# Kernel optimization log

Measured on AMD Instinct MI355X. Metric: run time of the kernel, lower is better.

Reference implementation:

```python
import jax, jax.numpy as jnp
import numpy as np

FLOW_NUM = 2048
H = 64  # lstm_output_dim
NOISE_DIM = 3


def _w(key, shape, s=0.08):
    return (jax.random.normal(key, shape, dtype=jnp.float32) * s)


def setup_inputs() -> dict:
    key = jax.random.key(0)
    ks = jax.random.split(key, 20)
    d = {
        "noise": jax.random.normal(ks[0], (FLOW_NUM, NOISE_DIM), dtype=jnp.float32),
        "w_ih0": _w(ks[1], (4 * H, NOISE_DIM)),
        "w_hh0": _w(ks[2], (4 * H, H)),
        "b_ih0": _w(ks[3], (4 * H,)),
        "b_hh0": _w(ks[4], (4 * H,)),
        "w_ih1": _w(ks[5], (4 * H, H)),
        "w_hh1": _w(ks[6], (4 * H, H)),
        "b_ih1": _w(ks[7], (4 * H,)),
        "b_hh1": _w(ks[8], (4 * H,)),
        "w_ih2": _w(ks[9], (4 * H, H)),
        "w_hh2": _w(ks[10], (4 * H, H)),
        "b_ih2": _w(ks[11], (4 * H,)),
        "b_hh2": _w(ks[12], (4 * H,)),
        "fc1_w": _w(ks[13], (32, H)),
        "fc1_b": _w(ks[14], (32,)),
        "fc2_w": _w(ks[15], (16, 32)),
        "fc2_b": _w(ks[16], (16,)),
        "fc3_w": _w(ks[17], (3, 16)),
        "fc3_b": _w(ks[18], (3,)),
        "flow_length": 500,
    }
    return d


def _lstm_cell(x, h, c, w_ih, w_hh, b_ih, b_hh):
    # PyTorch gate order: input, forget, cell(g), output
    gates = x @ w_ih.T + h @ w_hh.T + (b_ih + b_hh)
    i, f, g, o = jnp.split(gates, 4, axis=-1)
    c_new = jax.nn.sigmoid(f) * c + jax.nn.sigmoid(i) * jnp.tanh(g)
    h_new = jax.nn.sigmoid(o) * jnp.tanh(c_new)
    return h_new, c_new


def reference(noise, w_ih0, w_hh0, b_ih0, b_hh0,
              w_ih1, w_hh1, b_ih1, b_hh1,
              w_ih2, w_hh2, b_ih2, b_hh2,
              fc1_w, fc1_b, fc2_w, fc2_b, fc3_w, fc3_b,
              flow_length):
    layers = [(w_ih0, w_hh0, b_ih0, b_hh0),
              (w_ih1, w_hh1, b_ih1, b_hh1),
              (w_ih2, w_hh2, b_ih2, b_hh2)]
    n = noise.shape[0]
    h0 = jnp.zeros((3, n, H), dtype=noise.dtype)
    c0 = jnp.zeros((3, n, H), dtype=noise.dtype)

    def step(carry, _):
        x, h, c = carry
        inp = x
        hs, cs = [], []
        for l, (wi, wh, bi, bh) in enumerate(layers):
            h_l, c_l = _lstm_cell(inp, h[l], c[l], wi, wh, bi, bh)
            hs.append(h_l)
            cs.append(c_l)
            inp = h_l
        # MLP head (Dropout is identity in eval mode); LeakyReLU slope 0.01
        y = jax.nn.leaky_relu(inp @ fc1_w.T + fc1_b)
        y = jax.nn.leaky_relu(y @ fc2_w.T + fc2_b)
        y = jax.nn.leaky_relu(y @ fc3_w.T + fc3_b)
        return (y, jnp.stack(hs), jnp.stack(cs)), y

    _, flow = jax.lax.scan(step, (noise, h0, c0), None, length=flow_length)
    # flow: [flow_length, flow_num, 3] -> [flow_num, flow_length, 3]
    return jnp.swapaxes(flow, 0, 1)
```

## Files before the change

### kernel.cpp

```cpp
#include <hip/hip_runtime.h>

#define NT 512

typedef _Float16 f16x8 __attribute__((ext_vector_type(8)));
typedef _Float16 f16x4 __attribute__((ext_vector_type(4)));
typedef float    f32x4 __attribute__((ext_vector_type(4)));

#define MFMA(a, b, c) __builtin_amdgcn_mfma_f32_16x16x32_f16((a), (b), (c), 0, 0, 0)

#if __has_builtin(__builtin_amdgcn_exp2f)
__device__ __forceinline__ float fexp(float x) { return __builtin_amdgcn_exp2f(x * 1.4426950408889634f); }
#else
__device__ __forceinline__ float fexp(float x) { return __expf(x); }
#endif
#if __has_builtin(__builtin_amdgcn_rcpf)
__device__ __forceinline__ float frcp(float x) { return __builtin_amdgcn_rcpf(x); }
#else
__device__ __forceinline__ float frcp(float x) { return 1.0f / x; }
#endif
__device__ __forceinline__ float sigm(float x)  { return frcp(1.0f + fexp(-x)); }
__device__ __forceinline__ float tanh_(float x) { return 1.0f - 2.0f * frcp(1.0f + fexp(2.0f * x)); }
__device__ __forceinline__ float lrelu(float x) { return x > 0.0f ? x : 0.01f * x; }

__device__ __forceinline__ f16x8 ld8(const float* p) {
    const float4* q = (const float4*)p;
    float4 a = q[0], b = q[1];
    f16x8 r = { (_Float16)a.x, (_Float16)a.y, (_Float16)a.z, (_Float16)a.w,
                (_Float16)b.x, (_Float16)b.y, (_Float16)b.z, (_Float16)b.w };
    return r;
}

__global__ __launch_bounds__(NT, 2)
void gen_kernel(
    const float* __restrict__ noise,
    const float* __restrict__ w_ih0, const float* __restrict__ w_hh0,
    const float* __restrict__ b_ih0, const float* __restrict__ b_hh0,
    const float* __restrict__ w_ih1, const float* __restrict__ w_hh1,
    const float* __restrict__ b_ih1, const float* __restrict__ b_hh1,
    const float* __restrict__ w_ih2, const float* __restrict__ w_hh2,
    const float* __restrict__ b_ih2, const float* __restrict__ b_hh2,
    const float* __restrict__ fc1_w, const float* __restrict__ fc1_b,
    const float* __restrict__ fc2_w, const float* __restrict__ fc2_b,
    const float* __restrict__ fc3_w, const float* __restrict__ fc3_b,
    const int*   __restrict__ flow_len_p,
    float* __restrict__ out)
{
    __shared__ _Float16 sh[3][2][16 * 64] __attribute__((aligned(16)));
    __shared__ _Float16 sx [16][40] __attribute__((aligned(16)));
    __shared__ _Float16 sy1[16][40] __attribute__((aligned(16)));
    __shared__ _Float16 sy2[16][40] __attribute__((aligned(16)));
    __shared__ float so[2][8][16][3] __attribute__((aligned(16)));

    const int tid  = threadIdx.x;
    const int l    = tid & 63;
    const int w    = tid >> 6;
    const int ls   = l & 15;
    const int lj   = l >> 4;
    const int base = blockIdx.x * 8;
    const int T    = flow_len_p[0];

    const int gA  = ls & 3;
    const int rA0 = gA * 64 + 4 * (2 * w + 0) + (ls >> 2);
    const int rA1 = gA * 64 + 4 * (2 * w + 1) + (ls >> 2);

    f16x8 A1[2][4], A2[2][4], A0[2][3];
#pragma unroll
    for (int kc = 0; kc < 2; ++kc) {
        A1[0][kc]     = ld8(w_ih1 + rA0 * 64 + 32 * kc + 8 * lj);
        A1[1][kc]     = ld8(w_ih1 + rA1 * 64 + 32 * kc + 8 * lj);
        A1[0][2 + kc] = ld8(w_hh1 + rA0 * 64 + 32 * kc + 8 * lj);
        A1[1][2 + kc] = ld8(w_hh1 + rA1 * 64 + 32 * kc + 8 * lj);
        A2[0][kc]     = ld8(w_ih2 + rA0 * 64 + 32 * kc + 8 * lj);
        A2[1][kc]     = ld8(w_ih2 + rA1 * 64 + 32 * kc + 8 * lj);
        A2[0][2 + kc] = ld8(w_hh2 + rA0 * 64 + 32 * kc + 8 * lj);
        A2[1][2 + kc] = ld8(w_hh2 + rA1 * 64 + 32 * kc + 8 * lj);
        A0[0][kc]     = ld8(w_hh0 + rA0 * 64 + 32 * kc + 8 * lj);
        A0[1][kc]     = ld8(w_hh0 + rA1 * 64 + 32 * kc + 8 * lj);
    }
#pragma unroll
    for (int tt = 0; tt < 2; ++tt) {
        const int r = tt ? rA1 : rA0;
        f16x8 v;
#pragma unroll
        for (int i = 0; i < 8; ++i) {
            int kl = 8 * lj + i;
            float x = (kl < 3) ? w_ih0[r * 3 + kl]
                    : (kl == 3) ? (b_ih0[r] + b_hh0[r]) : 0.0f;
            v[i] = (_Float16)x;
        }
        A0[tt][2] = v;
    }
    f16x8 F1[2][2], F2, F3;
#pragma unroll
    for (int tt = 0; tt < 2; ++tt)
#pragma unroll
        for (int kc = 0; kc < 2; ++kc)
            F1[tt][kc] = ld8(fc1_w + (16 * tt + ls) * 64 + 32 * kc + 8 * lj);
    F2 = ld8(fc2_w + ls * 32 + 8 * lj);
    {
        f16x8 v;
#pragma unroll
        for (int i = 0; i < 8; ++i) {
            int k = 8 * lj + i;
            v[i] = (_Float16)((ls < 3 && k < 16) ? fc3_w[ls * 16 + k] : 0.0f);
        }
        F3 = v;
    }
    const int uc0 = 8 * w + lj, uc1 = 8 * w + 4 + lj;
    const int u_own = (ls < 8) ? uc0 : uc1;
    const int cs    = ls & 7;
    const int whaddr = cs * 64 + 8 * (((u_own >> 3) + cs) & 7) + (u_own & 7);
    float b1o[4], b2o[4];
#pragma unroll
    for (int g = 0; g < 4; ++g) {
        b1o[g] = b_ih1[g * 64 + u_own] + b_hh1[g * 64 + u_own];
        b2o[g] = b_ih2[g * 64 + u_own] + b_hh2[g * 64 + u_own];
    }
    float hb1a[4], hb1b[4], hb2[4];
#pragma unroll
    for (int r = 0; r < 4; ++r) {
        hb1a[r] = fc1_b[4 * lj + r];
        hb1b[r] = fc1_b[16 + 4 * lj + r];
        hb2[r]  = fc2_b[4 * lj + r];
    }
    float fb3[3] = { fc3_b[0], fc3_b[1], fc3_b[2] };

    for (int i = tid; i < 3 * 2 * 16 * 64; i += NT) ((_Float16*)sh)[i] = (_Float16)0.0f;
    for (int i = tid; i < 16 * 40; i += NT) {
        ((_Float16*)sx)[i]  = (_Float16)0.0f;
        ((_Float16*)sy1)[i] = (_Float16)0.0f;
        ((_Float16*)sy2)[i] = (_Float16)0.0f;
    }
    __syncthreads();
    if (tid < 16) sx[tid][3] = (_Float16)1.0f;
    if (tid < 24) {
        int s = tid / 3, d = tid % 3;
        sx[s][d] = (_Float16)noise[(base + s) * 3 + d];
    }

    float c0s = 0.0f, c1s = 0.0f, c2s = 0.0f;
    const float zb[4] = {0, 0, 0, 0};
    __syncthreads();

#define RD(L, p, kg) (*(const f16x8*)&sh[L][p][ls * 64 + 8 * (((kg) + ls) & 7)])

#define REPACK(cell, a0, a1)                                                   \
    float cell[4];                                                             \
    _Pragma("unroll")                                                          \
    for (int r = 0; r < 4; ++r) {                                              \
        float v_ = __shfl_xor(a1[r], 8);                                       \
        cell[r] = (ls < 8) ? a0[r] : v_;                                       \
    }

#define ACTC(cell, bo, cref, L, p) {                                           \
        float gi = cell[0] + bo[0], gf = cell[1] + bo[1];                      \
        float gg = cell[2] + bo[2], go = cell[3] + bo[3];                      \
        cref = sigm(gf) * cref + sigm(gi) * tanh_(gg);                         \
        sh[L][p][whaddr] = (_Float16)(sigm(go) * tanh_(cref)); }

    {
        f16x8 bx = *(const f16x8*)&sx[ls][8 * lj];
        f32x4 a0 = {0, 0, 0, 0}, a1 = {0, 0, 0, 0};
        a0 = MFMA(A0[0][2], bx, a0);
        a1 = MFMA(A0[1][2], bx, a1);
        REPACK(cell, a0, a1)
        ACTC(cell, zb, c0s, 0, 0)
    }
    __syncthreads();
    f16x8 ph1a = RD(1, 1, lj), ph1b = RD(1, 1, 4 + lj);

    for (int t = 0; t < T; ++t) {
        const int pc = t & 1, pp = pc ^ 1;
        f16x8 r0 = RD(0, pc, lj), r1 = RD(0, pc, 4 + lj);
        f16x8 nh2a = RD(2, pp, lj), nh2b = RD(2, pp, 4 + lj);
        {
            f32x4 a0 = {0, 0, 0, 0}, a1 = {0, 0, 0, 0};
            a0 = MFMA(A1[0][0], r0, a0);   a1 = MFMA(A1[1][0], r0, a1);
            a0 = MFMA(A1[0][1], r1, a0);   a1 = MFMA(A1[1][1], r1, a1);
            a0 = MFMA(A1[0][2], ph1a, a0); a1 = MFMA(A1[1][2], ph1a, a1);
            a0 = MFMA(A1[0][3], ph1b, a0); a1 = MFMA(A1[1][3], ph1b, a1);
            REPACK(cell, a0, a1)
            ACTC(cell, b1o, c1s, 1, pc)
        }
        __syncthreads();
        {
            f16x8 s0 = RD(1, pc, lj), s1 = RD(1, pc, 4 + lj);
            f32x4 a0 = {0, 0, 0, 0}, a1 = {0, 0, 0, 0};
            a0 = MFMA(A2[0][0], s0, a0);   a1 = MFMA(A2[1][0], s0, a1);
            a0 = MFMA(A2[0][1], s1, a0);   a1 = MFMA(A2[1][1], s1, a1);
            a0 = MFMA(A2[0][2], nh2a, a0); a1 = MFMA(A2[1][2], nh2a, a1);
            a0 = MFMA(A2[0][3], nh2b, a0); a1 = MFMA(A2[1][3], nh2b, a1);
            REPACK(cell, a0, a1)
            ACTC(cell, b2o, c2s, 2, pc)
        }
        __syncthreads();
        f32x4 h0a = {0, 0, 0, 0}, h0b = {0, 0, 0, 0};
        h0a = MFMA(A0[0][0], r0, h0a); h0b = MFMA(A0[1][0], r0, h0b);
        h0a = MFMA(A0[0][1], r1, h0a); h0b = MFMA(A0[1][1], r1, h0b);
        if (w == 0) {
            f16x8 bh0 = RD(2, pc, lj), bh1 = RD(2, pc, 4 + lj);
            f32x4 y1a = {0, 0, 0, 0}, y1b = {0, 0, 0, 0};
            y1a = MFMA(F1[0][0], bh0, y1a); y1b = MFMA(F1[1][0], bh0, y1b);
            y1a = MFMA(F1[0][1], bh1, y1a); y1b = MFMA(F1[1][1], bh1, y1b);
            f16x4 v;
#pragma unroll
            for (int r = 0; r < 4; ++r) v[r] = (_Float16)lrelu(y1a[r] + hb1a[r]);
            *(f16x4*)&sy1[ls][4 * lj] = v;
#pragma unroll
            for (int r = 0; r < 4; ++r) v[r] = (_Float16)lrelu(y1b[r] + hb1b[r]);
            *(f16x4*)&sy1[ls][16 + 4 * lj] = v;
            f16x8 by1 = *(const f16x8*)&sy1[ls][8 * lj];
            f32x4 y2 = {0, 0, 0, 0};
            y2 = MFMA(F2, by1, y2);
#pragma unroll
            for (int r = 0; r < 4; ++r) v[r] = (_Float16)lrelu(y2[r] + hb2[r]);
            *(f16x4*)&sy2[ls][4 * lj] = v;
            f16x8 by2 = *(const f16x8*)&sy2[ls][8 * lj];
            f32x4 y3 = {0, 0, 0, 0};
            y3 = MFMA(F3, by2, y3);
            if (lj == 0) {
                float o0 = lrelu(y3[0] + fb3[0]);
                float o1 = lrelu(y3[1] + fb3[1]);
                float o2 = lrelu(y3[2] + fb3[2]);
                sx[ls][0] = (_Float16)o0;
                sx[ls][1] = (_Float16)o1;
                sx[ls][2] = (_Float16)o2;
                if (ls < 8) {
                    float* sp = &so[(t >> 4) & 1][ls][t & 15][0];
                    sp[0] = o0; sp[1] = o1; sp[2] = o2;
                }
            }
        }
        if (w == 7 && t >= 16 && (t & 15) == 0) {
            const int tb = t - 16, pb = (tb >> 4) & 1;
            for (int task = l; task < 96; task += 64) {
                int s = task / 12, c = task % 12;
                *(float4*)(out + ((size_t)(base + s) * T + tb) * 3 + 4 * c) =
                    *(const float4*)((const float*)&so[pb][s][0][0] + 4 * c);
            }
        }
        __syncthreads();
        {
            f16x8 bx = *(const f16x8*)&sx[ls][8 * lj];
            h0a = MFMA(A0[0][2], bx, h0a);
            h0b = MFMA(A0[1][2], bx, h0b);
            REPACK(cell, h0a, h0b)
            ACTC(cell, zb, c0s, 0, pp)
        }
        ph1a = RD(1, pc, lj); ph1b = RD(1, pc, 4 + lj);
        __syncthreads();
    }

    if (w == 7 && T > 0) {
        const int tf = ((T - 1) >> 4) << 4;
        const int pb = (tf >> 4) & 1;
        const int n  = T - tf;
        for (int task = l; task < n * 8 * 3; task += 64) {
            int s = task / (n * 3), r = task % (n * 3);
            int q = r / 3, d = r % 3;
            out[((size_t)(base + s) * T + tf + q) * 3 + d] = so[pb][s][q][d];
        }
    }
}

extern "C" void kernel_launch(void* const* d_in, const int* in_sizes, int n_in,
                              void* d_out, int out_size, void* d_ws, size_t ws_size,
                              hipStream_t stream) {
    const float* noise = (const float*)d_in[0];
    const float* w_ih0 = (const float*)d_in[1];
    const float* w_hh0 = (const float*)d_in[2];
    const float* b_ih0 = (const float*)d_in[3];
    const float* b_hh0 = (const float*)d_in[4];
    const float* w_ih1 = (const float*)d_in[5];
    const float* w_hh1 = (const float*)d_in[6];
    const float* b_ih1 = (const float*)d_in[7];
    const float* b_hh1 = (const float*)d_in[8];
    const float* w_ih2 = (const float*)d_in[9];
    const float* w_hh2 = (const float*)d_in[10];
    const float* b_ih2 = (const float*)d_in[11];
    const float* b_hh2 = (const float*)d_in[12];
    const float* fc1w  = (const float*)d_in[13];
    const float* fc1b  = (const float*)d_in[14];
    const float* fc2w  = (const float*)d_in[15];
    const float* fc2b  = (const float*)d_in[16];
    const float* fc3w  = (const float*)d_in[17];
    const float* fc3b  = (const float*)d_in[18];
    const int*   flp   = (const int*)d_in[19];

    gen_kernel<<<dim3(256), dim3(NT), 0, stream>>>(
        noise, w_ih0, w_hh0, b_ih0, b_hh0,
        w_ih1, w_hh1, b_ih1, b_hh1,
        w_ih2, w_hh2, b_ih2, b_hh2,
        fc1w, fc1b, fc2w, fc2b, fc3w, fc3b,
        flp, (float*)d_out);
}
```

Measured before the change: 806.3 us.

## Precompute recurrent MFMA partials early and pass MLP activations via shuffles

The recurrent-hidden contributions for layers 1 and 2 (h1·W_hh1, h2·W_hh2) are now computed in the previous step's slack phases and carried as accumulators. This shortens the critical-path MFMA chain before each layer's activation. The MLP head's intermediate activations are packed to fp16 and redistributed with cross-lane shuffles instead of round-tripping through shared memory, which removes LDS writes and reads. It costs more live registers and extra shuffles, and the timing of the partial sums must stay correct across the double buffers.

```diff
diff --git a/kernel.cpp b/kernel.cpp
--- a/kernel.cpp
+++ b/kernel.cpp
@@ -3,8 +3,8 @@
 #define NT 512
 
 typedef _Float16 f16x8 __attribute__((ext_vector_type(8)));
-typedef _Float16 f16x4 __attribute__((ext_vector_type(4)));
 typedef float    f32x4 __attribute__((ext_vector_type(4)));
+typedef unsigned u32x4 __attribute__((ext_vector_type(4)));
 
 #define MFMA(a, b, c) __builtin_amdgcn_mfma_f32_16x16x32_f16((a), (b), (c), 0, 0, 0)
 
@@ -28,6 +28,14 @@
     f16x8 r = { (_Float16)a.x, (_Float16)a.y, (_Float16)a.z, (_Float16)a.w,
                 (_Float16)b.x, (_Float16)b.y, (_Float16)b.z, (_Float16)b.w };
     return r;
+}
+
+__device__ __forceinline__ unsigned pkh(float a, float b) {
+    auto h = __builtin_amdgcn_cvt_pkrtz(a, b);
+    return __builtin_bit_cast(unsigned, h);
+}
+__device__ __forceinline__ unsigned shflu(unsigned v, int lane) {
+    return (unsigned)__shfl((int)v, lane, 64);
 }
 
 __global__ __launch_bounds__(NT, 2)
@@ -47,8 +55,6 @@
 {
     __shared__ _Float16 sh[3][2][16 * 64] __attribute__((aligned(16)));
     __shared__ _Float16 sx [16][40] __attribute__((aligned(16)));
-    __shared__ _Float16 sy1[16][40] __attribute__((aligned(16)));
-    __shared__ _Float16 sy2[16][40] __attribute__((aligned(16)));
     __shared__ float so[2][8][16][3] __attribute__((aligned(16)));
 
     const int tid  = threadIdx.x;
@@ -125,12 +131,11 @@
     }
     float fb3[3] = { fc3_b[0], fc3_b[1], fc3_b[2] };
 
+    const int s01 = ls + 16 * ((2 * lj) & 3);
+    const int s23 = ls + 16 * ((2 * lj + 1) & 3);
+
     for (int i = tid; i < 3 * 2 * 16 * 64; i += NT) ((_Float16*)sh)[i] = (_Float16)0.0f;
-    for (int i = tid; i < 16 * 40; i += NT) {
-        ((_Float16*)sx)[i]  = (_Float16)0.0f;
-        ((_Float16*)sy1)[i] = (_Float16)0.0f;
-        ((_Float16*)sy2)[i] = (_Float16)0.0f;
-    }
+    for (int i = tid; i < 16 * 40; i += NT) ((_Float16*)sx)[i] = (_Float16)0.0f;
     __syncthreads();
     if (tid < 16) sx[tid][3] = (_Float16)1.0f;
     if (tid < 24) {
@@ -140,6 +145,7 @@
 
     float c0s = 0.0f, c1s = 0.0f, c2s = 0.0f;
     const float zb[4] = {0, 0, 0, 0};
+    const f32x4 z4 = {0, 0, 0, 0};
     __syncthreads();
 
 #define RD(L, p, kg) (*(const f16x8*)&sh[L][p][ls * 64 + 8 * (((kg) + ls) & 7)])
@@ -160,63 +166,68 @@
 
     {
         f16x8 bx = *(const f16x8*)&sx[ls][8 * lj];
-        f32x4 a0 = {0, 0, 0, 0}, a1 = {0, 0, 0, 0};
+        f32x4 a0 = z4, a1 = z4;
         a0 = MFMA(A0[0][2], bx, a0);
         a1 = MFMA(A0[1][2], bx, a1);
         REPACK(cell, a0, a1)
         ACTC(cell, zb, c0s, 0, 0)
     }
     __syncthreads();
-    f16x8 ph1a = RD(1, 1, lj), ph1b = RD(1, 1, 4 + lj);
+
+    f32x4 u0 = z4, u1 = z4, p0 = z4, p1 = z4;
 
     for (int t = 0; t < T; ++t) {
         const int pc = t & 1, pp = pc ^ 1;
         f16x8 r0 = RD(0, pc, lj), r1 = RD(0, pc, 4 + lj);
-        f16x8 nh2a = RD(2, pp, lj), nh2b = RD(2, pp, 4 + lj);
         {
-            f32x4 a0 = {0, 0, 0, 0}, a1 = {0, 0, 0, 0};
-            a0 = MFMA(A1[0][0], r0, a0);   a1 = MFMA(A1[1][0], r0, a1);
-            a0 = MFMA(A1[0][1], r1, a0);   a1 = MFMA(A1[1][1], r1, a1);
-            a0 = MFMA(A1[0][2], ph1a, a0); a1 = MFMA(A1[1][2], ph1a, a1);
-            a0 = MFMA(A1[0][3], ph1b, a0); a1 = MFMA(A1[1][3], ph1b, a1);
+            f32x4 v0 = z4, v1 = z4;
+            v0 = MFMA(A1[0][0], r0, v0);   v1 = MFMA(A1[1][0], r0, v1);
+            v0 = MFMA(A1[0][1], r1, v0);   v1 = MFMA(A1[1][1], r1, v1);
+            f32x4 a0 = u0 + v0, a1 = u1 + v1;
             REPACK(cell, a0, a1)
             ACTC(cell, b1o, c1s, 1, pc)
         }
         __syncthreads();
+        f16x8 s0 = RD(1, pc, lj), s1 = RD(1, pc, 4 + lj);
         {
-            f16x8 s0 = RD(1, pc, lj), s1 = RD(1, pc, 4 + lj);
-            f32x4 a0 = {0, 0, 0, 0}, a1 = {0, 0, 0, 0};
-            a0 = MFMA(A2[0][0], s0, a0);   a1 = MFMA(A2[1][0], s0, a1);
-            a0 = MFMA(A2[0][1], s1, a0);   a1 = MFMA(A2[1][1], s1, a1);
-            a0 = MFMA(A2[0][2], nh2a, a0); a1 = MFMA(A2[1][2], nh2a, a1);
-            a0 = MFMA(A2[0][3], nh2b, a0); a1 = MFMA(A2[1][3], nh2b, a1);
+            f32x4 q0 = z4, q1 = z4;
+            q0 = MFMA(A2[0][0], s0, q0);   q1 = MFMA(A2[1][0], s0, q1);
+            q0 = MFMA(A2[0][1], s1, q0);   q1 = MFMA(A2[1][1], s1, q1);
+            f32x4 a0 = p0 + q0, a1 = p1 + q1;
             REPACK(cell, a0, a1)
             ACTC(cell, b2o, c2s, 2, pc)
         }
         __syncthreads();
-        f32x4 h0a = {0, 0, 0, 0}, h0b = {0, 0, 0, 0};
+        f16x8 nh2a = RD(2, pc, lj), nh2b = RD(2, pc, 4 + lj);
+        f32x4 h0a = z4, h0b = z4;
         h0a = MFMA(A0[0][0], r0, h0a); h0b = MFMA(A0[1][0], r0, h0b);
         h0a = MFMA(A0[0][1], r1, h0a); h0b = MFMA(A0[1][1], r1, h0b);
+        p0 = MFMA(A2[0][2], nh2a, z4); p1 = MFMA(A2[1][2], nh2a, z4);
+        p0 = MFMA(A2[0][3], nh2b, p0); p1 = MFMA(A2[1][3], nh2b, p1);
         if (w == 0) {
-            f16x8 bh0 = RD(2, pc, lj), bh1 = RD(2, pc, 4 + lj);
-            f32x4 y1a = {0, 0, 0, 0}, y1b = {0, 0, 0, 0};
-            y1a = MFMA(F1[0][0], bh0, y1a); y1b = MFMA(F1[1][0], bh0, y1b);
-            y1a = MFMA(F1[0][1], bh1, y1a); y1b = MFMA(F1[1][1], bh1, y1b);
-            f16x4 v;
-#pragma unroll
-            for (int r = 0; r < 4; ++r) v[r] = (_Float16)lrelu(y1a[r] + hb1a[r]);
-            *(f16x4*)&sy1[ls][4 * lj] = v;
-#pragma unroll
-            for (int r = 0; r < 4; ++r) v[r] = (_Float16)lrelu(y1b[r] + hb1b[r]);
-            *(f16x4*)&sy1[ls][16 + 4 * lj] = v;
-            f16x8 by1 = *(const f16x8*)&sy1[ls][8 * lj];
-            f32x4 y2 = {0, 0, 0, 0};
+            f32x4 y1a = z4, y1b = z4;
+            y1a = MFMA(F1[0][0], nh2a, y1a); y1b = MFMA(F1[1][0], nh2a, y1b);
+            y1a = MFMA(F1[0][1], nh2b, y1a); y1b = MFMA(F1[1][1], nh2b, y1b);
+            unsigned pa0 = pkh(lrelu(y1a[0] + hb1a[0]), lrelu(y1a[1] + hb1a[1]));
+            unsigned pa1 = pkh(lrelu(y1a[2] + hb1a[2]), lrelu(y1a[3] + hb1a[3]));
+            unsigned pb0 = pkh(lrelu(y1b[0] + hb1b[0]), lrelu(y1b[1] + hb1b[1]));
+            unsigned pb1 = pkh(lrelu(y1b[2] + hb1b[2]), lrelu(y1b[3] + hb1b[3]));
+            unsigned t0a = shflu(pa0, s01), t0b = shflu(pb0, s01);
+            unsigned t1a = shflu(pa1, s01), t1b = shflu(pb1, s01);
+            unsigned t2a = shflu(pa0, s23), t2b = shflu(pb0, s23);
+            unsigned t3a = shflu(pa1, s23), t3b = shflu(pb1, s23);
+            const bool lo = (lj < 2);
+            u32x4 B1 = { lo ? t0a : t0b, lo ? t1a : t1b, lo ? t2a : t2b, lo ? t3a : t3b };
+            f16x8 by1 = __builtin_bit_cast(f16x8, B1);
+            f32x4 y2 = z4;
             y2 = MFMA(F2, by1, y2);
-#pragma unroll
-            for (int r = 0; r < 4; ++r) v[r] = (_Float16)lrelu(y2[r] + hb2[r]);
-            *(f16x4*)&sy2[ls][4 * lj] = v;
-            f16x8 by2 = *(const f16x8*)&sy2[ls][8 * lj];
-            f32x4 y3 = {0, 0, 0, 0};
+            unsigned q0 = pkh(lrelu(y2[0] + hb2[0]), lrelu(y2[1] + hb2[1]));
+            unsigned q1 = pkh(lrelu(y2[2] + hb2[2]), lrelu(y2[3] + hb2[3]));
+            unsigned z0 = shflu(q0, s01), z1 = shflu(q1, s01);
+            unsigned z2 = shflu(q0, s23), z3 = shflu(q1, s23);
+            u32x4 B2 = { z0, z1, z2, z3 };
+            f16x8 by2 = __builtin_bit_cast(f16x8, B2);
+            f32x4 y3 = z4;
             y3 = MFMA(F3, by2, y3);
             if (lj == 0) {
                 float o0 = lrelu(y3[0] + fb3[0]);
@@ -242,12 +253,13 @@
         __syncthreads();
         {
             f16x8 bx = *(const f16x8*)&sx[ls][8 * lj];
+            u0 = MFMA(A1[0][2], s0, z4); u1 = MFMA(A1[1][2], s0, z4);
+            u0 = MFMA(A1[0][3], s1, u0); u1 = MFMA(A1[1][3], s1, u1);
             h0a = MFMA(A0[0][2], bx, h0a);
             h0b = MFMA(A0[1][2], bx, h0b);
             REPACK(cell, h0a, h0b)
             ACTC(cell, zb, c0s, 0, pp)
         }
-        ph1a = RD(1, pc, lj); ph1b = RD(1, pc, 4 + lj);
         __syncthreads();
     }
 
```

Result: slower. 858.4 us (+6.5%).
